# Kernel optimization log

Hardware: AMD Instinct MI355X
Metric: run time of the kernel (lower is better)

The kernel has to match this reference:

```python
import jax, jax.numpy as jnp
import numpy as np

NEG_SLOPE = 0.2  # PyG GATConv default negative_slope
N_NODES = 40000
N_EDGES = 640000
IN_DIM = 128
SAT_DIM = 64
HID = 128
OUT_DIM = 54


def gat_conv(x, edge_index, W, a_src, a_dst, bias):
    """PyG GATConv with heads=1, concat=True, add_self_loops=True."""
    n = x.shape[0]
    loops = jnp.arange(n, dtype=edge_index.dtype)
    src = jnp.concatenate([edge_index[0], loops])  # message sources j
    dst = jnp.concatenate([edge_index[1], loops])  # message targets i
    h = x @ W.T                                    # [N, C]
    alpha_s = h @ a_src                            # [N]
    alpha_d = h @ a_dst                            # [N]
    e = jax.nn.leaky_relu(alpha_s[src] + alpha_d[dst], NEG_SLOPE)  # [E]
    # segment softmax over incoming edges of each dst node (self-loops guarantee non-empty segments)
    m = jax.ops.segment_max(e, dst, num_segments=n)
    e = jnp.exp(e - m[dst])
    denom = jax.ops.segment_sum(e, dst, num_segments=n)
    alpha = e / (denom[dst] + 1e-16)
    out = jax.ops.segment_sum(alpha[:, None] * h[src], dst, num_segments=n)
    return out + bias


def setup_inputs() -> dict:
    key = jax.random.key(0)
    ks = jax.random.split(key, 16)
    s = lambda d: 1.0 / np.sqrt(d)
    inp = {
        "x": jax.random.normal(ks[0], (N_NODES, IN_DIM), jnp.float32),
        "edge_index": jax.random.randint(ks[1], (2, N_EDGES), 0, N_NODES, jnp.int32),
        "sat_W": jax.random.normal(ks[2], (HID, SAT_DIM), jnp.float32) * s(SAT_DIM),
        "sat_b": jnp.zeros((HID,), jnp.float32),
        "neigh_W": jax.random.normal(ks[3], (HID, IN_DIM - SAT_DIM), jnp.float32) * s(IN_DIM - SAT_DIM),
        "neigh_b": jnp.zeros((HID,), jnp.float32),
        "conv1_W": jax.random.normal(ks[4], (HID, HID), jnp.float32) * s(HID),
        "conv1_asrc": jax.random.normal(ks[5], (HID,), jnp.float32) * s(HID),
        "conv1_adst": jax.random.normal(ks[6], (HID,), jnp.float32) * s(HID),
        "conv1_b": jnp.zeros((HID,), jnp.float32),
        "conv2_W": jax.random.normal(ks[7], (HID, HID), jnp.float32) * s(HID),
        "conv2_asrc": jax.random.normal(ks[8], (HID,), jnp.float32) * s(HID),
        "conv2_adst": jax.random.normal(ks[9], (HID,), jnp.float32) * s(HID),
        "conv2_b": jnp.zeros((HID,), jnp.float32),
        "fc1_W": jax.random.normal(ks[10], (HID, HID), jnp.float32) * s(HID),
        "fc1_b": jnp.zeros((HID,), jnp.float32),
        "fc2_W": jax.random.normal(ks[11], (OUT_DIM, HID), jnp.float32) * s(HID),
        "fc2_b": jnp.zeros((OUT_DIM,), jnp.float32),
    }
    return inp


def reference(x, edge_index, sat_W, sat_b, neigh_W, neigh_b,
              conv1_W, conv1_asrc, conv1_adst, conv1_b,
              conv2_W, conv2_asrc, conv2_adst, conv2_b,
              fc1_W, fc1_b, fc2_W, fc2_b):
    sat = jax.nn.relu(x[:, :SAT_DIM] @ sat_W.T + sat_b)
    nei = jax.nn.relu(x[:, SAT_DIM:] @ neigh_W.T + neigh_b)
    h = sat + 0.5 * nei
    h = jax.nn.relu(gat_conv(h, edge_index, conv1_W, conv1_asrc, conv1_adst, conv1_b))
    h = jax.nn.relu(gat_conv(h, edge_index, conv2_W, conv2_asrc, conv2_adst, conv2_b))
    h = jax.nn.relu(h @ fc1_W.T + fc1_b)
    return h @ fc2_W.T + fc2_b
```

## Files before the change

kernel.cpp:

```cpp
#include <hip/hip_runtime.h>


#define N_NODES 40000
#define N_EDGES 640000
#define DIM     128

typedef unsigned short u16;
typedef __attribute__((ext_vector_type(8))) short bf16x8;
typedef __attribute__((ext_vector_type(4))) float f32x4;

#define GLOAD_LDS16(GSRC, LDST)                                                \
    __builtin_amdgcn_global_load_lds(                                          \
        (const __attribute__((address_space(1))) void*)(GSRC),                 \
        (__attribute__((address_space(3))) void*)(LDST), 16, 0, 0)

__device__ __forceinline__ u16 f2bf(float v) {
    unsigned u = __float_as_uint(v);
    u += 0x7FFFu + ((u >> 16) & 1u);
    return (u16)(u >> 16);
}
__device__ __forceinline__ float bf2f(u16 h) { return __uint_as_float(((unsigned)h) << 16); }
__device__ __forceinline__ float rdlane_f(float v, int l) {
    return __uint_as_float(__builtin_amdgcn_readlane(__float_as_uint(v), l));
}

__device__ __forceinline__ int hswz(int row, int col) {
    return row * 128 + ((((col >> 2) ^ (row & 7))) << 2) + (col & 3);
}
__device__ __forceinline__ float4 hread4(const float* hbuf, int row, int k) {
    int b = (k >> 2) ^ (row & 7);
    return *(const float4*)&hbuf[row * 128 + (b << 2)];
}
__device__ __forceinline__ void split8(const float* vv, bf16x8& hi, bf16x8& lo) {
#pragma unroll
    for (int i = 0; i < 8; ++i) {
        u16 h = f2bf(vv[i]);
        hi[i] = (short)h;
        lo[i] = (short)f2bf(vv[i] - bf2f(h));
    }
}

#define MFMA3(ACC, AH, AL, BH, BL)                                             \
    ACC = __builtin_amdgcn_mfma_f32_16x16x32_bf16(AH, BH, ACC, 0, 0, 0);       \
    ACC = __builtin_amdgcn_mfma_f32_16x16x32_bf16(AH, BL, ACC, 0, 0, 0);       \
    ACC = __builtin_amdgcn_mfma_f32_16x16x32_bf16(AL, BH, ACC, 0, 0, 0);

__global__ __launch_bounds__(256) void k_wcvt(
    const float* __restrict__ satW, const float* __restrict__ neiW,
    const float* __restrict__ c1W, const float* __restrict__ c2W,
    const float* __restrict__ f1W, const float* __restrict__ f2W,
    u16* __restrict__ wa, int* __restrict__ deg, int* __restrict__ counter) {
    int gid = (blockIdx.y * gridDim.x + blockIdx.x) * 256 + threadIdx.x;
    if (gid < N_NODES) deg[gid] = 1;
    if (gid == 0) *counter = 0;

    int m = blockIdx.y;
    const float* src; int C, K, Cp; int offH, offL;
    switch (m) {
        case 0: src = satW; C = 128; K = 64;  Cp = 128; offH = 0;      offL = 8192;   break;
        case 1: src = neiW; C = 128; K = 64;  Cp = 128; offH = 16384;  offL = 24576;  break;
        case 2: src = c1W;  C = 128; K = 128; Cp = 128; offH = 32768;  offL = 49152;  break;
        case 3: src = c2W;  C = 128; K = 128; Cp = 128; offH = 65536;  offL = 81920;  break;
        case 4: src = f1W;  C = 128; K = 128; Cp = 128; offH = 98304;  offL = 114688; break;
        default:src = f2W;  C = 54;  K = 128; Cp = 64;  offH = 131072; offL = 139264; break;
    }
    int e = blockIdx.x * 256 + threadIdx.x;
    if (e >= Cp * K) return;
    int c = e / K, k = e - c * K;
    float v = (c < C) ? src[c * K + k] : 0.f;
    u16 h = f2bf(v);
    wa[offH + e] = h;
    wa[offL + e] = f2bf(v - bf2f(h));
}

__global__ void k_deg_count(const int* __restrict__ dst, int* __restrict__ deg) {
    int t = blockIdx.x * 256 + threadIdx.x;
    if (t < N_EDGES) atomicAdd(&deg[dst[t]], 1);
}
__global__ void k_assign(const int* __restrict__ deg, int* __restrict__ counter,
                         int* __restrict__ start, int* __restrict__ cursor,
                         int* __restrict__ csr_src) {
    int i = blockIdx.x * 256 + threadIdx.x;
    if (i >= N_NODES) return;
    int d = deg[i];
    int s = atomicAdd(counter, d);
    start[i] = s;
    csr_src[s] = i;
    cursor[i] = s + 1;
}
__global__ void k_fill_edges(const int* __restrict__ src, const int* __restrict__ dst,
                             int* __restrict__ cursor, int* __restrict__ csr_src) {
    int t = blockIdx.x * 256 + threadIdx.x;
    if (t < N_EDGES) {
        int p = atomicAdd(&cursor[dst[t]], 1);
        csr_src[p] = src[t];
    }
}

template<int CT>
__device__ __forceinline__ void stage_W(u16* Ws, const u16* __restrict__ Wh,
                                        const u16* __restrict__ Wl, int kc, int tid) {
    for (int idx = tid; idx < CT * 2 * 2 * 64; idx += 256) {
        int l = idx & 63;
        int q = idx >> 6;
        int hilo = q & 1;
        int ks = (q >> 1) & 1;
        int ct = q >> 2;
        int c = ct * 16 + (l & 15);
        int k = kc * 64 + ks * 32 + (l >> 4) * 8;
        const u16* Wp = hilo ? Wl : Wh;
        GLOAD_LDS16(Wp + (size_t)c * 128 + k, &Ws[idx * 8]);
    }
}
__device__ __forceinline__ void stage_W64(u16* Ws, const u16* __restrict__ Wh,
                                          const u16* __restrict__ Wl, int tid) {
    for (int idx = tid; idx < 2048; idx += 256) {
        int l = idx & 63;
        int q = idx >> 6;
        int hilo = q & 1;
        int ks = (q >> 1) & 1;
        int ct = q >> 2;
        int c = ct * 16 + (l & 15);
        int k = ks * 32 + (l >> 4) * 8;
        const u16* Wp = hilo ? Wl : Wh;
        GLOAD_LDS16(Wp + (size_t)c * 64 + k, &Ws[idx * 8]);
    }
}

__device__ __forceinline__ void alpha_epi(const f32x4* acc, int lane, int r0,
                                          const float* __restrict__ a_src,
                                          const float* __restrict__ a_dst,
                                          float* __restrict__ as_, float* __restrict__ ad_) {
    float ps[4] = {0, 0, 0, 0}, pd[4] = {0, 0, 0, 0};
#pragma unroll
    for (int ct = 0; ct < 8; ++ct) {
        float asv = a_src[ct * 16 + (lane & 15)];
        float adv = a_dst[ct * 16 + (lane & 15)];
#pragma unroll
        for (int r = 0; r < 4; ++r) {
            ps[r] = fmaf(acc[ct][r], asv, ps[r]);
            pd[r] = fmaf(acc[ct][r], adv, pd[r]);
        }
    }
#pragma unroll
    for (int off = 1; off < 16; off <<= 1) {
#pragma unroll
        for (int r = 0; r < 4; ++r) {
            ps[r] += __shfl_xor(ps[r], off);
            pd[r] += __shfl_xor(pd[r], off);
        }
    }
    if ((lane & 15) == 0) {
#pragma unroll
        for (int r = 0; r < 4; ++r) {
            int row = r0 + (lane >> 4) * 4 + r;
            as_[row] = ps[r];
            ad_[row] = pd[r];
        }
    }
}

__global__ __launch_bounds__(256) void k_enc_conv1(
    const float* __restrict__ x,
    const u16* __restrict__ sH, const u16* __restrict__ sL,
    const u16* __restrict__ nH, const u16* __restrict__ nL,
    const float* __restrict__ satb, const float* __restrict__ neib,
    const u16* __restrict__ Wh, const u16* __restrict__ Wl,
    const float* __restrict__ a_src, const float* __restrict__ a_dst,
    u16* __restrict__ outG, float* __restrict__ as_, float* __restrict__ ad_)
{
    __shared__ u16 WbufA[16384];
    __shared__ u16 WbufB[16384];
    float* hbuf = (float*)WbufA;
    const int tid = threadIdx.x, lane = tid & 63, wv = tid >> 6;
    const int r0 = blockIdx.x * 64 + wv * 16;
    const int arow = r0 + (lane & 15);
    const int kb = (lane >> 4) * 8;

    stage_W<8>(WbufB, Wh, Wl, 0, tid);
    stage_W64(WbufA, sH, sL, tid);

    bf16x8 axh[4], axl[4];
#pragma unroll
    for (int s = 0; s < 4; ++s) {
        const float* p = x + (size_t)arow * 128 + s * 32 + kb;
        float4 a = *(const float4*)p;
        float4 b = *(const float4*)(p + 4);
        float vv[8] = {a.x, a.y, a.z, a.w, b.x, b.y, b.z, b.w};
        split8(vv, axh[s], axl[s]);
    }

    f32x4 accS[8], accN[8];
#pragma unroll
    for (int ct = 0; ct < 8; ++ct) { accS[ct] = (f32x4){0,0,0,0}; accN[ct] = (f32x4){0,0,0,0}; }

    __syncthreads();
#pragma unroll
    for (int ct = 0; ct < 8; ++ct) {
#pragma unroll
        for (int ks = 0; ks < 2; ++ks) {
            int base = (ct * 2 + ks) * 1024;
            bf16x8 bh = *reinterpret_cast<const bf16x8*>(&WbufA[base + lane * 8]);
            bf16x8 bl = *reinterpret_cast<const bf16x8*>(&WbufA[base + 512 + lane * 8]);
            MFMA3(accS[ct], axh[ks], axl[ks], bh, bl);
        }
    }
    __syncthreads();
    stage_W64(WbufA, nH, nL, tid);
    __syncthreads();
#pragma unroll
    for (int ct = 0; ct < 8; ++ct) {
#pragma unroll
        for (int ks = 0; ks < 2; ++ks) {
            int base = (ct * 2 + ks) * 1024;
            bf16x8 bh = *reinterpret_cast<const bf16x8*>(&WbufA[base + lane * 8]);
            bf16x8 bl = *reinterpret_cast<const bf16x8*>(&WbufA[base + 512 + lane * 8]);
            MFMA3(accN[ct], axh[ks + 2], axl[ks + 2], bh, bl);
        }
    }
    __syncthreads();

#pragma unroll
    for (int ct = 0; ct < 8; ++ct) {
        int c = ct * 16 + (lane & 15);
        float bs = satb[c], bn = neib[c];
#pragma unroll
        for (int r = 0; r < 4; ++r) {
            int rl = wv * 16 + (lane >> 4) * 4 + r;
            float v = fmaxf(accS[ct][r] + bs, 0.f) + 0.5f * fmaxf(accN[ct][r] + bn, 0.f);
            hbuf[hswz(rl, c)] = v;
        }
    }
    __syncthreads();

    bf16x8 ah[4], al[4];
    const int ar = wv * 16 + (lane & 15);
#pragma unroll
    for (int s = 0; s < 4; ++s) {
        int k0 = s * 32 + kb;
        float4 a = hread4(hbuf, ar, k0);
        float4 b = hread4(hbuf, ar, k0 + 4);
        float vv[8] = {a.x, a.y, a.z, a.w, b.x, b.y, b.z, b.w};
        split8(vv, ah[s], al[s]);
    }
    __syncthreads();

    stage_W<8>(WbufA, Wh, Wl, 1, tid);

    f32x4 acc[8];
#pragma unroll
    for (int ct = 0; ct < 8; ++ct) acc[ct] = (f32x4){0, 0, 0, 0};
#pragma unroll
    for (int ct = 0; ct < 8; ++ct) {
#pragma unroll
        for (int ks = 0; ks < 2; ++ks) {
            int base = (ct * 2 + ks) * 1024;
            bf16x8 bh = *reinterpret_cast<const bf16x8*>(&WbufB[base + lane * 8]);
            bf16x8 bl = *reinterpret_cast<const bf16x8*>(&WbufB[base + 512 + lane * 8]);
            MFMA3(acc[ct], ah[ks], al[ks], bh, bl);
        }
    }
    __syncthreads();
#pragma unroll
    for (int ct = 0; ct < 8; ++ct) {
#pragma unroll
        for (int ks = 0; ks < 2; ++ks) {
            int base = (ct * 2 + ks) * 1024;
            bf16x8 bh = *reinterpret_cast<const bf16x8*>(&WbufA[base + lane * 8]);
            bf16x8 bl = *reinterpret_cast<const bf16x8*>(&WbufA[base + 512 + lane * 8]);
            MFMA3(acc[ct], ah[2 + ks], al[2 + ks], bh, bl);
        }
    }

    alpha_epi(acc, lane, r0, a_src, a_dst, as_, ad_);

#pragma unroll
    for (int ct = 0; ct < 8; ++ct) {
        int c = ct * 16 + (lane & 15);
#pragma unroll
        for (int r = 0; r < 4; ++r) {
            int row = r0 + (lane >> 4) * 4 + r;
            outG[(size_t)row * 128 + c] = f2bf(acc[ct][r]);
        }
    }
}

__global__ __launch_bounds__(256) void k_conv_gemm(
    const u16* __restrict__ Ah, const u16* __restrict__ Al,
    const u16* __restrict__ Wh, const u16* __restrict__ Wl,
    const float* __restrict__ a_src, const float* __restrict__ a_dst,
    u16* __restrict__ outG, float* __restrict__ as_, float* __restrict__ ad_)
{
    __shared__ u16 WbufA[16384];
    __shared__ u16 WbufB[16384];
    const int tid = threadIdx.x, lane = tid & 63, wv = tid >> 6;
    const int r0 = blockIdx.x * 64 + wv * 16;
    const int arow = r0 + (lane & 15);
    const int kb = (lane >> 4) * 8;

    stage_W<8>(WbufA, Wh, Wl, 0, tid);
    stage_W<8>(WbufB, Wh, Wl, 1, tid);

    bf16x8 ah[4], al[4];
#pragma unroll
    for (int s = 0; s < 4; ++s) {
        ah[s] = *reinterpret_cast<const bf16x8*>(Ah + (size_t)arow * 128 + s * 32 + kb);
        al[s] = *reinterpret_cast<const bf16x8*>(Al + (size_t)arow * 128 + s * 32 + kb);
    }

    f32x4 acc[8];
#pragma unroll
    for (int ct = 0; ct < 8; ++ct) acc[ct] = (f32x4){0, 0, 0, 0};

    __syncthreads();
#pragma unroll
    for (int ct = 0; ct < 8; ++ct) {
#pragma unroll
        for (int ks = 0; ks < 2; ++ks) {
            int base = (ct * 2 + ks) * 1024;
            bf16x8 bh = *reinterpret_cast<const bf16x8*>(&WbufA[base + lane * 8]);
            bf16x8 bl = *reinterpret_cast<const bf16x8*>(&WbufA[base + 512 + lane * 8]);
            MFMA3(acc[ct], ah[ks], al[ks], bh, bl);
            bf16x8 ch = *reinterpret_cast<const bf16x8*>(&WbufB[base + lane * 8]);
            bf16x8 cl = *reinterpret_cast<const bf16x8*>(&WbufB[base + 512 + lane * 8]);
            MFMA3(acc[ct], ah[2 + ks], al[2 + ks], ch, cl);
        }
    }

    alpha_epi(acc, lane, r0, a_src, a_dst, as_, ad_);

#pragma unroll
    for (int ct = 0; ct < 8; ++ct) {
        int c = ct * 16 + (lane & 15);
#pragma unroll
        for (int r = 0; r < 4; ++r) {
            int row = r0 + (lane >> 4) * 4 + r;
            outG[(size_t)row * 128 + c] = f2bf(acc[ct][r]);
        }
    }
}

__global__ __launch_bounds__(256) void k_fc12(
    const u16* __restrict__ Ah, const u16* __restrict__ Al,
    const u16* __restrict__ W1h, const u16* __restrict__ W1l, const float* __restrict__ b1,
    const u16* __restrict__ W2h, const u16* __restrict__ W2l, const float* __restrict__ b2,
    float* __restrict__ out)
{
    __shared__ u16 WbufA[16384];
    __shared__ u16 WbufB[16384];
    float* hbuf = (float*)WbufA;
    const int tid = threadIdx.x, lane = tid & 63, wv = tid >> 6;
    const int r0 = blockIdx.x * 64 + wv * 16;
    const int arow = r0 + (lane & 15);
    const int kb = (lane >> 4) * 8;

    stage_W<4>(WbufB, W2h, W2l, 0, tid);
    stage_W<4>(WbufB + 8192, W2h, W2l, 1, tid);
    stage_W<8>(WbufA, W1h, W1l, 0, tid);

    bf16x8 ah[4], al[4];
#pragma unroll
    for (int s = 0; s < 4; ++s) {
        ah[s] = *reinterpret_cast<const bf16x8*>(Ah + (size_t)arow * 128 + s * 32 + kb);
        al[s] = *reinterpret_cast<const bf16x8*>(Al + (size_t)arow * 128 + s * 32 + kb);
    }

    f32x4 acc[8];
#pragma unroll
    for (int ct = 0; ct < 8; ++ct) acc[ct] = (f32x4){0, 0, 0, 0};

    __syncthreads();
#pragma unroll
    for (int ct = 0; ct < 8; ++ct) {
#pragma unroll
        for (int ks = 0; ks < 2; ++ks) {
            int base = (ct * 2 + ks) * 1024;
            bf16x8 bh = *reinterpret_cast<const bf16x8*>(&WbufA[base + lane * 8]);
            bf16x8 bl = *reinterpret_cast<const bf16x8*>(&WbufA[base + 512 + lane * 8]);
            MFMA3(acc[ct], ah[ks], al[ks], bh, bl);
        }
    }
    __syncthreads();
    stage_W<8>(WbufA, W1h, W1l, 1, tid);
    __syncthreads();
#pragma unroll
    for (int ct = 0; ct < 8; ++ct) {
#pragma unroll
        for (int ks = 0; ks < 2; ++ks) {
            int base = (ct * 2 + ks) * 1024;
            bf16x8 bh = *reinterpret_cast<const bf16x8*>(&WbufA[base + lane * 8]);
            bf16x8 bl = *reinterpret_cast<const bf16x8*>(&WbufA[base + 512 + lane * 8]);
            MFMA3(acc[ct], ah[2 + ks], al[2 + ks], bh, bl);
        }
    }
    __syncthreads();

#pragma unroll
    for (int ct = 0; ct < 8; ++ct) {
        int c = ct * 16 + (lane & 15);
        float bv = b1[c];
#pragma unroll
        for (int r = 0; r < 4; ++r) {
            int rl = wv * 16 + (lane >> 4) * 4 + r;
            hbuf[hswz(rl, c)] = fmaxf(acc[ct][r] + bv, 0.f);
        }
    }
    __syncthreads();

    bf16x8 a2h[4], a2l[4];
    const int ar = wv * 16 + (lane & 15);
#pragma unroll
    for (int s = 0; s < 4; ++s) {
        int k0 = s * 32 + kb;
        float4 a = hread4(hbuf, ar, k0);
        float4 b = hread4(hbuf, ar, k0 + 4);
        float vv[8] = {a.x, a.y, a.z, a.w, b.x, b.y, b.z, b.w};
        split8(vv, a2h[s], a2l[s]);
    }

    f32x4 acc2[4];
#pragma unroll
    for (int ct = 0; ct < 4; ++ct) acc2[ct] = (f32x4){0, 0, 0, 0};
#pragma unroll
    for (int kc = 0; kc < 2; ++kc) {
        const u16* Wb = WbufB + kc * 8192;
#pragma unroll
        for (int ct = 0; ct < 4; ++ct) {
#pragma unroll
            for (int ks = 0; ks < 2; ++ks) {
                int s = kc * 2 + ks;
                int base = (ct * 2 + ks) * 1024;
                bf16x8 bh = *reinterpret_cast<const bf16x8*>(&Wb[base + lane * 8]);
                bf16x8 bl = *reinterpret_cast<const bf16x8*>(&Wb[base + 512 + lane * 8]);
                MFMA3(acc2[ct], a2h[s], a2l[s], bh, bl);
            }
        }
    }

#pragma unroll
    for (int ct = 0; ct < 4; ++ct) {
        int c = ct * 16 + (lane & 15);
#pragma unroll
        for (int r = 0; r < 4; ++r) {
            int row = r0 + (lane >> 4) * 4 + r;
            if (c < 54) out[(size_t)row * 54 + c] = acc2[ct][r] + b2[c];
        }
    }
}

#define DO_PAIRS(NP, TB)                                                      \
    {                                                                         \
        float pw[NP]; const ushort4* hp[NP];                                  \
        _Pragma("unroll")                                                     \
        for (int q = 0; q < NP; ++q) {                                        \
            int e0 = (TB) + 2 * q;                                            \
            float plo = rdlane_f(p, e0), phi = rdlane_f(p, e0 + 1);           \
            int jlo = __builtin_amdgcn_readlane(jj, e0);                      \
            int jhi = __builtin_amdgcn_readlane(jj, e0 + 1);                  \
            pw[q] = hodd ? phi : plo;                                         \
            int j = hodd ? jhi : jlo;                                         \
            hp[q] = (const ushort4*)&hg[(size_t)j * 128 + 4 * l32];           \
        }                                                                     \
        ushort4 hv[NP];                                                       \
        _Pragma("unroll") for (int q = 0; q < NP; ++q) hv[q] = *hp[q];        \
        _Pragma("unroll") for (int q = 0; q < NP; ++q) {                      \
            acc.x = fmaf(pw[q], bf2f(hv[q].x), acc.x);                        \
            acc.y = fmaf(pw[q], bf2f(hv[q].y), acc.y);                        \
            acc.z = fmaf(pw[q], bf2f(hv[q].z), acc.z);                        \
            acc.w = fmaf(pw[q], bf2f(hv[q].w), acc.w);                        \
        }                                                                     \
    }

__global__ __launch_bounds__(256) void k_aggregate(
    const u16* __restrict__ hg, const float* __restrict__ as_,
    const float* __restrict__ ad_, const int* __restrict__ start,
    const int* __restrict__ deg, const int* __restrict__ csr_src,
    const float* __restrict__ bias, u16* __restrict__ outH, u16* __restrict__ outL)
{
    int wid = (blockIdx.x * 256 + threadIdx.x) >> 6;
    int lane = threadIdx.x & 63;
    if (wid >= N_NODES) return;

    const int s0 = start[wid];
    const int s1 = s0 + deg[wid];
    const float adi = ad_[wid];
    const int l32 = lane & 31;
    const bool hodd = lane >= 32;

    float4 acc = make_float4(0.f, 0.f, 0.f, 0.f);
    float ssum = 0.f;
    for (int base = s0; base < s1; base += 64) {
        int k = base + lane;
        int cnt = min(64, s1 - base);
        int jj = 0;
        float p = 0.f;
        if (k < s1) {
            jj = csr_src[k];
            float e = as_[jj] + adi;
            e = (e > 0.f) ? e : 0.2f * e;
            p = __expf(e);
            ssum += p;
        }
        int t = 0;
        for (; t + 16 <= cnt; t += 16) DO_PAIRS(8, t)
        if (t + 8 <= cnt) { DO_PAIRS(4, t) t += 8; }
        if (t + 4 <= cnt) { DO_PAIRS(2, t) t += 4; }
        for (; t < cnt; t += 2) DO_PAIRS(1, t)
    }
#pragma unroll
    for (int off = 32; off; off >>= 1) ssum += __shfl_xor(ssum, off);
    acc.x += __shfl_xor(acc.x, 32);
    acc.y += __shfl_xor(acc.y, 32);
    acc.z += __shfl_xor(acc.z, 32);
    acc.w += __shfl_xor(acc.w, 32);
    float inv = 1.f / (ssum + 1e-16f);

    if (!hodd) {
        float4 bv = *(const float4*)&bias[4 * l32];
        float o0 = fmaxf(fmaf(acc.x, inv, bv.x), 0.f);
        float o1 = fmaxf(fmaf(acc.y, inv, bv.y), 0.f);
        float o2 = fmaxf(fmaf(acc.z, inv, bv.z), 0.f);
        float o3 = fmaxf(fmaf(acc.w, inv, bv.w), 0.f);
        u16 h0 = f2bf(o0), h1 = f2bf(o1), h2 = f2bf(o2), h3 = f2bf(o3);
        ushort4 hvv = make_ushort4(h0, h1, h2, h3);
        ushort4 lvv = make_ushort4(f2bf(o0 - bf2f(h0)), f2bf(o1 - bf2f(h1)),
                                   f2bf(o2 - bf2f(h2)), f2bf(o3 - bf2f(h3)));
        *(ushort4*)&outH[(size_t)wid * 128 + 4 * l32] = hvv;
        *(ushort4*)&outL[(size_t)wid * 128 + 4 * l32] = lvv;
    }
}

extern "C" void kernel_launch(void* const* d_in, const int* in_sizes, int n_in,
                              void* d_out, int out_size, void* d_ws, size_t ws_size,
                              hipStream_t stream) {
    (void)in_sizes; (void)n_in; (void)out_size; (void)ws_size;

    const float* x       = (const float*)d_in[0];
    const int*   ei      = (const int*)d_in[1];
    const float* sat_W   = (const float*)d_in[2];
    const float* sat_b   = (const float*)d_in[3];
    const float* neigh_W = (const float*)d_in[4];
    const float* neigh_b = (const float*)d_in[5];
    const float* c1_W    = (const float*)d_in[6];
    const float* c1_as   = (const float*)d_in[7];
    const float* c1_ad   = (const float*)d_in[8];
    const float* c1_b    = (const float*)d_in[9];
    const float* c2_W    = (const float*)d_in[10];
    const float* c2_as   = (const float*)d_in[11];
    const float* c2_ad   = (const float*)d_in[12];
    const float* c2_b    = (const float*)d_in[13];
    const float* fc1_W   = (const float*)d_in[14];
    const float* fc1_b   = (const float*)d_in[15];
    const float* fc2_W   = (const float*)d_in[16];
    const float* fc2_b   = (const float*)d_in[17];

    const int* e_src = ei;
    const int* e_dst = ei + N_EDGES;

    char* w = (char*)d_ws;
    u16*   hG     = (u16*)  (w);
    u16*   hH     = (u16*)  (w + 10240000);
    u16*   hL     = (u16*)  (w + 20480000);
    float* as_    = (float*)(w + 30720000);
    float* ad_    = (float*)(w + 30880000);
    int*   deg    = (int*)  (w + 31040000);
    int*   start  = (int*)  (w + 31200000);
    int*   cursor = (int*)  (w + 31360000);
    int*   counter= (int*)  (w + 31520000);
    int*   csr    = (int*)  (w + 31520256);
    u16*   wa     = (u16*)  (w + 34240256);

    u16 *satH = wa,          *satL = wa + 8192;
    u16 *neiH = wa + 16384,  *neiL = wa + 24576;
    u16 *c1H  = wa + 32768,  *c1L  = wa + 49152;
    u16 *c2H  = wa + 65536,  *c2L  = wa + 81920;
    u16 *f1H  = wa + 98304,  *f1L  = wa + 114688;
    u16 *f2H  = wa + 131072, *f2L  = wa + 139264;

    dim3 b(256);
    k_wcvt<<<dim3(64, 6), b, 0, stream>>>(sat_W, neigh_W, c1_W, c2_W, fc1_W, fc2_W,
                                          wa, deg, counter);
    k_deg_count <<<2500, b, 0, stream>>>(e_dst, deg);
    k_assign    <<<157,  b, 0, stream>>>(deg, counter, start, cursor, csr);
    k_fill_edges<<<2500, b, 0, stream>>>(e_src, e_dst, cursor, csr);

    k_enc_conv1<<<625, b, 0, stream>>>(x, satH, satL, neiH, neiL, sat_b, neigh_b,
                                       c1H, c1L, c1_as, c1_ad, hG, as_, ad_);
    k_aggregate<<<10000, b, 0, stream>>>(hG, as_, ad_, start, deg, csr, c1_b, hH, hL);

    k_conv_gemm<<<625, b, 0, stream>>>(hH, hL, c2H, c2L, c2_as, c2_ad, hG, as_, ad_);
    k_aggregate<<<10000, b, 0, stream>>>(hG, as_, ad_, start, deg, csr, c2_b, hH, hL);

    k_fc12<<<625, b, 0, stream>>>(hH, hL, f1H, f1L, fc1_b, f2H, f2L, fc2_b,
                                  (float*)d_out);
}
```

Before: 205.2 us.

## Use single shared weight buffer in encoder+conv1 kernel to cut LDS usage

```diff
diff --git a/kernel.cpp b/kernel.cpp
--- a/kernel.cpp
+++ b/kernel.cpp
@@ -169,16 +169,12 @@
     const float* __restrict__ a_src, const float* __restrict__ a_dst,
     u16* __restrict__ outG, float* __restrict__ as_, float* __restrict__ ad_)
 {
-    __shared__ u16 WbufA[16384];
-    __shared__ u16 WbufB[16384];
-    float* hbuf = (float*)WbufA;
+    __shared__ u16 Wbuf[16384];
+    float* hbuf = (float*)Wbuf;
     const int tid = threadIdx.x, lane = tid & 63, wv = tid >> 6;
     const int r0 = blockIdx.x * 64 + wv * 16;
     const int arow = r0 + (lane & 15);
     const int kb = (lane >> 4) * 8;
-
-    stage_W<8>(WbufB, Wh, Wl, 0, tid);
-    stage_W64(WbufA, sH, sL, tid);
 
     bf16x8 axh[4], axl[4];
 #pragma unroll
@@ -194,28 +190,22 @@
 #pragma unroll
     for (int ct = 0; ct < 8; ++ct) { accS[ct] = (f32x4){0,0,0,0}; accN[ct] = (f32x4){0,0,0,0}; }
 
-    __syncthreads();
-#pragma unroll
-    for (int ct = 0; ct < 8; ++ct) {
-#pragma unroll
-        for (int ks = 0; ks < 2; ++ks) {
-            int base = (ct * 2 + ks) * 1024;
-            bf16x8 bh = *reinterpret_cast<const bf16x8*>(&WbufA[base + lane * 8]);
-            bf16x8 bl = *reinterpret_cast<const bf16x8*>(&WbufA[base + 512 + lane * 8]);
-            MFMA3(accS[ct], axh[ks], axl[ks], bh, bl);
-        }
-    }
-    __syncthreads();
-    stage_W64(WbufA, nH, nL, tid);
-    __syncthreads();
-#pragma unroll
-    for (int ct = 0; ct < 8; ++ct) {
-#pragma unroll
-        for (int ks = 0; ks < 2; ++ks) {
-            int base = (ct * 2 + ks) * 1024;
-            bf16x8 bh = *reinterpret_cast<const bf16x8*>(&WbufA[base + lane * 8]);
-            bf16x8 bl = *reinterpret_cast<const bf16x8*>(&WbufA[base + 512 + lane * 8]);
-            MFMA3(accN[ct], axh[ks + 2], axl[ks + 2], bh, bl);
+#pragma unroll
+    for (int mat = 0; mat < 2; ++mat) {
+        if (mat) __syncthreads();
+        stage_W64(Wbuf, mat ? nH : sH, mat ? nL : sL, tid);
+        __syncthreads();
+#pragma unroll
+        for (int ct = 0; ct < 8; ++ct) {
+#pragma unroll
+            for (int ks = 0; ks < 2; ++ks) {
+                int s = mat * 2 + ks;
+                int base = (ct * 2 + ks) * 1024;
+                bf16x8 bh = *reinterpret_cast<const bf16x8*>(&Wbuf[base + lane * 8]);
+                bf16x8 bl = *reinterpret_cast<const bf16x8*>(&Wbuf[base + 512 + lane * 8]);
+                f32x4* ac = mat ? &accN[ct] : &accS[ct];
+                MFMA3((*ac), axh[s], axl[s], bh, bl);
+            }
         }
     }
     __syncthreads();
@@ -245,30 +235,24 @@
     }
     __syncthreads();
 
-    stage_W<8>(WbufA, Wh, Wl, 1, tid);
-
     f32x4 acc[8];
 #pragma unroll
     for (int ct = 0; ct < 8; ++ct) acc[ct] = (f32x4){0, 0, 0, 0};
 #pragma unroll
-    for (int ct = 0; ct < 8; ++ct) {
-#pragma unroll
-        for (int ks = 0; ks < 2; ++ks) {
-            int base = (ct * 2 + ks) * 1024;
-            bf16x8 bh = *reinterpret_cast<const bf16x8*>(&WbufB[base + lane * 8]);
-            bf16x8 bl = *reinterpret_cast<const bf16x8*>(&WbufB[base + 512 + lane * 8]);
-            MFMA3(acc[ct], ah[ks], al[ks], bh, bl);
-        }
-    }
-    __syncthreads();
-#pragma unroll
-    for (int ct = 0; ct < 8; ++ct) {
-#pragma unroll
-        for (int ks = 0; ks < 2; ++ks) {
-            int base = (ct * 2 + ks) * 1024;
-            bf16x8 bh = *reinterpret_cast<const bf16x8*>(&WbufA[base + lane * 8]);
-            bf16x8 bl = *reinterpret_cast<const bf16x8*>(&WbufA[base + 512 + lane * 8]);
-            MFMA3(acc[ct], ah[2 + ks], al[2 + ks], bh, bl);
+    for (int kc = 0; kc < 2; ++kc) {
+        if (kc) __syncthreads();
+        stage_W<8>(Wbuf, Wh, Wl, kc, tid);
+        __syncthreads();
+#pragma unroll
+        for (int ct = 0; ct < 8; ++ct) {
+#pragma unroll
+            for (int ks = 0; ks < 2; ++ks) {
+                int s = kc * 2 + ks;
+                int base = (ct * 2 + ks) * 1024;
+                bf16x8 bh = *reinterpret_cast<const bf16x8*>(&Wbuf[base + lane * 8]);
+                bf16x8 bl = *reinterpret_cast<const bf16x8*>(&Wbuf[base + 512 + lane * 8]);
+                MFMA3(acc[ct], ah[s], al[s], bh, bl);
+            }
         }
     }
 
```

Result: no change. 203.0 us (-1.1%).
